# Kernel tuning notes

Measured on AMD Instinct MI355X. Metric: run time of the kernel, lower is better.

The kernel has to match this reference:

```python
import jax, jax.numpy as jnp
import numpy as np

N = 12000          # num nodes
H = 32             # hidden_dim
T = 50             # num_time_steps


def setup_inputs() -> dict:
    key = jax.random.key(0)
    k1, k2, k3, k4, k5 = jax.random.split(key, 5)
    t = jax.random.uniform(k1, (1,), dtype=jnp.float32)
    z = jax.random.normal(k2, (N, H), dtype=jnp.float32)
    # dense (row-normalized-ish) adjacency used by the GCN aggregation
    adj = jax.random.uniform(k3, (N, N), dtype=jnp.float32) / N
    treatments = jax.random.uniform(k4, (N, T, 1), dtype=jnp.float32)
    W = jax.random.normal(k5, (H + 1, H), dtype=jnp.float32) / np.sqrt(H + 1)
    b = jnp.zeros((H,), dtype=jnp.float32)
    return {"t": t, "z": z, "adj": adj, "treatments": treatments, "W": W, "b": b}


def reference(t, z, adj, treatments, W, b):
    # a_index = int(t * (num_time_steps - 1))
    a_idx = jnp.clip((t[0] * (T - 1)).astype(jnp.int32), 0, T - 1)
    a_t = jax.lax.dynamic_index_in_dim(treatments, a_idx, axis=1, keepdims=False)  # [N, 1]
    z_cat = jnp.concatenate([z, a_t], axis=1)                                      # [N, H+1]
    # GCN layer: relu(adj @ (x @ W) + b)
    support = z_cat @ W                                                            # [N, H]
    grad = jax.nn.relu(adj @ support + b)                                          # [N, H]
    return grad
```

## Files before the change

kernel.cpp:

```cpp
#include <hip/hip_runtime.h>

#define NN 12000
#define HH 32
#define TT 50
#define BM 96

typedef float f32x4 __attribute__((ext_vector_type(4)));

__global__ void support_kernel(const float* __restrict__ tt,
                               const float* __restrict__ z,
                               const float* __restrict__ treat,
                               const float* __restrict__ W,
                               float* __restrict__ support) {
  int tid = blockIdx.x * blockDim.x + threadIdx.x;
  if (tid >= NN * HH) return;
  int row = tid >> 5;
  int col = tid & 31;
  int aidx = (int)(tt[0] * (float)(TT - 1));
  aidx = aidx < 0 ? 0 : (aidx > TT - 1 ? TT - 1 : aidx);
  float at = treat[row * TT + aidx];
  float acc = at * W[HH * HH + col];
  const float* zr = z + row * HH;
#pragma unroll
  for (int k = 0; k < HH; ++k) acc = fmaf(zr[k], W[k * HH + col], acc);
  support[tid] = acc;
}

__global__ __launch_bounds__(256, 8) void spmm_kernel(
    const float* __restrict__ adj,
    const float* __restrict__ support,
    float* __restrict__ partial,
    int kper) {
  const int rb = blockIdx.x;
  const int s = blockIdx.y;
  const int tid = threadIdx.x;
  const int cg = tid & 7;
  const int rg = tid >> 3;
  const int k0 = s * kper;

  const f32x4* arow0 = (const f32x4*)(adj + (size_t)(rb * BM + rg) * NN + k0);
  const f32x4* arow1 =
      (const f32x4*)(adj + (size_t)(rb * BM + rg + 32) * NN + k0);
  const f32x4* arow2 =
      (const f32x4*)(adj + (size_t)(rb * BM + rg + 64) * NN + k0);
  const f32x4* bptr = ((const f32x4*)support) + (size_t)k0 * (HH / 4) + cg;

  f32x4 acc0 = (f32x4)0.f, acc1 = (f32x4)0.f, acc2 = (f32x4)0.f;

  const int nk4 = kper >> 2;
  for (int k4 = 0; k4 < nk4; ++k4) {
    f32x4 b0 = bptr[0 * (HH / 4)];
    f32x4 b1 = bptr[1 * (HH / 4)];
    f32x4 b2 = bptr[2 * (HH / 4)];
    f32x4 b3 = bptr[3 * (HH / 4)];
    f32x4 a0 = arow0[k4];
    f32x4 a1 = arow1[k4];
    f32x4 a2 = arow2[k4];
#define ROW_FMA(ACC, A)               \
    ACC += A.x * b0; ACC += A.y * b1; \
    ACC += A.z * b2; ACC += A.w * b3;
    ROW_FMA(acc0, a0)
    ROW_FMA(acc1, a1)
    ROW_FMA(acc2, a2)
#undef ROW_FMA
    bptr += 4 * (HH / 4);
  }

  f32x4* pout = (f32x4*)partial;
  const size_t sbase = (size_t)s * NN;
  pout[(sbase + rb * BM + rg) * (HH / 4) + cg] = acc0;
  pout[(sbase + rb * BM + rg + 32) * (HH / 4) + cg] = acc1;
  pout[(sbase + rb * BM + rg + 64) * (HH / 4) + cg] = acc2;
}

__global__ void combine_kernel(const float* __restrict__ partial,
                               const float* __restrict__ bias,
                               float* __restrict__ out, int splits) {
  int tid = blockIdx.x * blockDim.x + threadIdx.x;
  if (tid >= NN * HH / 4) return;
  int c0 = (tid & (HH / 4 - 1)) * 4;
  f32x4 acc = *(const f32x4*)(bias + c0);
  for (int s = 0; s < splits; ++s)
    acc += ((const f32x4*)partial)[(size_t)s * (NN * HH / 4) + tid];
  acc.x = fmaxf(acc.x, 0.f);
  acc.y = fmaxf(acc.y, 0.f);
  acc.z = fmaxf(acc.z, 0.f);
  acc.w = fmaxf(acc.w, 0.f);
  ((f32x4*)out)[tid] = acc;
}

extern "C" void kernel_launch(void* const* d_in, const int* in_sizes, int n_in,
                              void* d_out, int out_size, void* d_ws,
                              size_t ws_size, hipStream_t stream) {
  const float* t = (const float*)d_in[0];
  const float* z = (const float*)d_in[1];
  const float* adj = (const float*)d_in[2];
  const float* treat = (const float*)d_in[3];
  const float* W = (const float*)d_in[4];
  const float* b = (const float*)d_in[5];
  float* out = (float*)d_out;

  const size_t elem = (size_t)NN * HH;
  static const int split_opts[] = {15, 12, 10, 8, 6, 5, 4, 3, 2, 1};
  int splits = 1;
  for (int i = 0; i < 10; ++i) {
    if ((size_t)(split_opts[i] + 1) * elem * 4 <= ws_size) {
      splits = split_opts[i];
      break;
    }
  }
  const int kper = NN / splits;

  float* support = (float*)d_ws;
  float* partial = support + elem;

  support_kernel<<<(NN * HH + 255) / 256, 256, 0, stream>>>(t, z, treat, W,
                                                            support);
  dim3 grid(NN / BM, splits);
  spmm_kernel<<<grid, 256, 0, stream>>>(adj, support, partial, kper);
  combine_kernel<<<(NN * HH / 4 + 255) / 256, 256, 0, stream>>>(partial, b, out,
                                                                splits);
}
```

Before: 971.0 us.

## Stage support chunks into LDS via async global_load_lds with register-prefetched adj rows

```diff
diff --git a/kernel.cpp b/kernel.cpp
--- a/kernel.cpp
+++ b/kernel.cpp
@@ -4,6 +4,8 @@
 #define HH 32
 #define TT 50
 #define BM 96
+#define KC 160
+#define CHUNK_BYTES (KC * HH * 4)
 
 typedef float f32x4 __attribute__((ext_vector_type(4)));
 
@@ -26,45 +28,81 @@
   support[tid] = acc;
 }
 
-__global__ __launch_bounds__(256, 8) void spmm_kernel(
+__global__ __launch_bounds__(256, 4) void spmm_kernel(
     const float* __restrict__ adj,
     const float* __restrict__ support,
     float* __restrict__ partial,
     int kper) {
+  __shared__ __align__(16) float ldsb[2][KC * HH];
+
   const int rb = blockIdx.x;
   const int s = blockIdx.y;
   const int tid = threadIdx.x;
   const int cg = tid & 7;
   const int rg = tid >> 3;
+  const int wave = tid >> 6;
+  const int lane = tid & 63;
   const int k0 = s * kper;
+  const int nchunk = kper / KC;
+  const int nk4 = kper >> 2;
 
   const f32x4* arow0 = (const f32x4*)(adj + (size_t)(rb * BM + rg) * NN + k0);
   const f32x4* arow1 =
       (const f32x4*)(adj + (size_t)(rb * BM + rg + 32) * NN + k0);
   const f32x4* arow2 =
       (const f32x4*)(adj + (size_t)(rb * BM + rg + 64) * NN + k0);
-  const f32x4* bptr = ((const f32x4*)support) + (size_t)k0 * (HH / 4) + cg;
+  const char* gsrc =
+      (const char*)(support + (size_t)k0 * HH) + wave * 1024 + lane * 16;
+
+#define STAGE(buf, c)                                                        \
+  {                                                                          \
+    const char* gp = gsrc + (size_t)(c)*CHUNK_BYTES;                         \
+    char* lp = (char*)&ldsb[buf][0] + wave * 1024;                           \
+    _Pragma("unroll") for (int r = 0; r < CHUNK_BYTES / 4096; ++r)           \
+        __builtin_amdgcn_global_load_lds(                                    \
+            (const __attribute__((address_space(1))) unsigned int*)(gp +     \
+                                                                    r * 4096), \
+            (__attribute__((address_space(3))) unsigned int*)(lp + r * 4096), \
+            16, 0, 0);                                                       \
+  }
+
+  f32x4 aP0 = arow0[0], aP1 = arow1[0], aP2 = arow2[0];
+  f32x4 aQ0 = arow0[1], aQ1 = arow1[1], aQ2 = arow2[1];
+
+  STAGE(0, 0);
+  __syncthreads();
 
   f32x4 acc0 = (f32x4)0.f, acc1 = (f32x4)0.f, acc2 = (f32x4)0.f;
-
-  const int nk4 = kper >> 2;
-  for (int k4 = 0; k4 < nk4; ++k4) {
-    f32x4 b0 = bptr[0 * (HH / 4)];
-    f32x4 b1 = bptr[1 * (HH / 4)];
-    f32x4 b2 = bptr[2 * (HH / 4)];
-    f32x4 b3 = bptr[3 * (HH / 4)];
-    f32x4 a0 = arow0[k4];
-    f32x4 a1 = arow1[k4];
-    f32x4 a2 = arow2[k4];
+  int kk = 0;
+  int cur = 0;
+  for (int c = 0; c < nchunk; ++c) {
+    if (c + 1 < nchunk) STAGE(cur ^ 1, c + 1);
+    const float* bl = &ldsb[cur][0];
+#pragma unroll 2
+    for (int k4 = 0; k4 < KC / 4; ++k4) {
+      const f32x4* bp = ((const f32x4*)(bl + (k4 << 7))) + cg;
+      f32x4 b0 = bp[0];
+      f32x4 b1 = bp[8];
+      f32x4 b2 = bp[16];
+      f32x4 b3 = bp[24];
+      int kn = kk + 2;
+      kn = kn < nk4 ? kn : nk4 - 1;
+      f32x4 aN0 = arow0[kn], aN1 = arow1[kn], aN2 = arow2[kn];
 #define ROW_FMA(ACC, A)               \
-    ACC += A.x * b0; ACC += A.y * b1; \
-    ACC += A.z * b2; ACC += A.w * b3;
-    ROW_FMA(acc0, a0)
-    ROW_FMA(acc1, a1)
-    ROW_FMA(acc2, a2)
+      ACC += A.x * b0; ACC += A.y * b1; \
+      ACC += A.z * b2; ACC += A.w * b3;
+      ROW_FMA(acc0, aP0)
+      ROW_FMA(acc1, aP1)
+      ROW_FMA(acc2, aP2)
 #undef ROW_FMA
-    bptr += 4 * (HH / 4);
+      aP0 = aQ0; aP1 = aQ1; aP2 = aQ2;
+      aQ0 = aN0; aQ1 = aN1; aQ2 = aN2;
+      ++kk;
+    }
+    __syncthreads();
+    cur ^= 1;
   }
+#undef STAGE
 
   f32x4* pout = (f32x4*)partial;
   const size_t sbase = (size_t)s * NN;
@@ -101,9 +139,9 @@
   float* out = (float*)d_out;
 
   const size_t elem = (size_t)NN * HH;
-  static const int split_opts[] = {15, 12, 10, 8, 6, 5, 4, 3, 2, 1};
+  static const int split_opts[] = {15, 5, 3, 1};
   int splits = 1;
-  for (int i = 0; i < 10; ++i) {
+  for (int i = 0; i < 4; ++i) {
     if ((size_t)(split_opts[i] + 1) * elem * 4 <= ws_size) {
       splits = split_opts[i];
       break;
```

New measurement: 854.7 us. 12.0% less time.
